# Optimization experiments

Hardware: AMD Instinct MI355X
Metric: run time of the kernel (lower is better)

The kernel has to match this reference:

```python
import jax, jax.numpy as jnp
import numpy as np

B, N_IN, D, K, N = 8, 256, 128, 1024, 4096
EMA_GAMMA = 0.99


def setup_inputs() -> dict:
    key = jax.random.key(0)
    k1, k2, k3 = jax.random.split(key, 3)
    z = jax.random.normal(k1, (B, N_IN, N), dtype=jnp.float32)
    # Conv1d(n_in, d, 1, bias=False) == a (d, n_in) matmul; xavier-ish scale
    W_lin = jax.random.normal(k2, (D, N_IN), dtype=jnp.float32) * (1.0 / np.sqrt(N_IN))
    # codebook initialized xavier_uniform with gain=10 in the original
    lim = 10.0 * np.sqrt(6.0 / (K + D))
    emb = jax.random.uniform(k3, (K, D), dtype=jnp.float32, minval=-lim, maxval=lim)
    ema_numer = emb * (1.0 - EMA_GAMMA)
    ema_denom = jnp.ones((K,), dtype=jnp.float32) * (1.0 - EMA_GAMMA)
    return {"z": z, "W_lin": W_lin, "emb": emb,
            "ema_numer": ema_numer, "ema_denom": ema_denom}


def reference(z, W_lin, emb, ema_numer, ema_denom):
    # ze: (B, d, N) -- 1x1 conv == channel matmul
    ze = jnp.einsum('bcn,dc->bdn', z, W_lin)
    sg_emb = jax.lax.stop_gradient(emb)           # codebook is stop-gradded

    # scaled L2 distance:  ||ze - q|| / (||ze|| + ||q||), shape (B, K, N)
    ze_sq = jnp.sum(ze * ze, axis=1)              # (B, N)
    q_sq = jnp.sum(sg_emb * sg_emb, axis=1)       # (K,)
    dots = jnp.einsum('bdn,kd->bkn', ze, sg_emb)  # (B, K, N)
    dist_sq = jnp.maximum(ze_sq[:, None, :] + q_sq[None, :, None] - 2.0 * dots, 0.0)
    den = jnp.sqrt(ze_sq)[:, None, :] + jnp.sqrt(q_sq)[None, :, None]
    snorm = jnp.sqrt(dist_sq) / den               # (B, K, N)

    min_ind = jnp.argmin(snorm, axis=1)           # (B, N) int
    zq = jnp.moveaxis(sg_emb[min_ind], -1, 1)     # (B, d, N)

    # ReplaceGrad: forward value = zq, gradient routed to ze (straight-through)
    zq_rg = ze + jax.lax.stop_gradient(zq - ze)

    # EMA codebook statistics (scatter-add over codebook indices)
    flat_ind = min_ind.reshape(-1)                             # (B*N,)
    ze_flat = jax.lax.stop_gradient(
        jnp.moveaxis(ze, 1, 2).reshape(-1, ze.shape[1]))       # (B*N, d)
    z_sum = jax.ops.segment_sum(ze_flat, flat_ind, num_segments=K)   # (K, d)
    n_sum = jax.ops.segment_sum(jnp.ones(flat_ind.shape, ze.dtype),
                                flat_ind, num_segments=K)            # (K,)
    ema_numer_new = EMA_GAMMA * ema_numer + (1.0 - EMA_GAMMA) * z_sum
    ema_denom_new = EMA_GAMMA * ema_denom + (1.0 - EMA_GAMMA) * n_sum
    return zq_rg, ema_numer_new, ema_denom_new
```

## Files before the change

### kernel.cpp

```cpp
#include <hip/hip_runtime.h>
#include <cmath>
#include <stdint.h>

#define B_    8
#define NIN_  256
#define D_    128
#define K_    1024
#define N_    4096
#define P_    (B_ * N_)
#define MARGIN_M 1e-4f

typedef __attribute__((ext_vector_type(8))) short bf16x8;
typedef __attribute__((ext_vector_type(4))) float f32x4;

#define WS_ZSUM   0
#define WS_CNT    524288
#define WS_FLAGC  528384
#define WS_MEMSET 532480
#define WS_OFF    532480
#define WS_QSQ    536576
#define WS_QNORM  540672
#define WS_KSTAR  544768
#define WS_RANK   675840
#define WS_PLIST  806912
#define WS_KLIST  937984
#define WS_FLIST  1069056
#define WS_WT     1200128
#define WS_ZPM    1331200
#define WS_ZESQ   18108416
#define WS_ZEN    18239488
#define WS_ZE2F   18370560
#define WS_EMB2F  43536384
#define WS_VAL1   44322816
#define WS_IDX1   46419968
#define WS_VAL2   48517120

__device__ inline unsigned short f2bf(float v) {
  union { float f; uint32_t u; } c; c.f = v;
  return (unsigned short)((c.u + 0x7FFFu + ((c.u >> 16) & 1u)) >> 16);
}
__device__ inline float bf2f(unsigned short b) {
  union { float f; uint32_t u; } c; c.u = ((uint32_t)b) << 16; return c.f;
}
__device__ inline uint32_t pack2(float a, float b, int lo) {
  unsigned short ha = f2bf(a); if (lo) ha = f2bf(a - bf2f(ha));
  unsigned short hb = f2bf(b); if (lo) hb = f2bf(b - bf2f(hb));
  return (uint32_t)ha | ((uint32_t)hb << 16);
}

__global__ __launch_bounds__(256) void prep_kernel(
    const float* __restrict__ W, const float* __restrict__ emb,
    float* __restrict__ Wt, float* __restrict__ q_sq, float* __restrict__ q_norm,
    uint4* __restrict__ emb2f)
{
  const int tid = threadIdx.x;
  const int bid = blockIdx.x;
  if (bid < 128) {
    int t = bid * 256 + tid;
    int c = t >> 7, d = t & 127;
    Wt[t] = W[d * NIN_ + c];
  } else if (bid < 132) {
    int k = (bid - 128) * 256 + tid;
    const float* e = emb + (size_t)k * D_;
    float s = 0.f;
    #pragma unroll 8
    for (int d = 0; d < D_; ++d) s = fmaf(e[d], e[d], s);
    q_sq[k] = s;
    q_norm[k] = sqrtf(s);
  } else {
    const int kt = bid - 132;
    #pragma unroll
    for (int i = 0; i < 3; ++i) {
      int f    = i * 256 + tid;
      int c    = f >> 6;
      int lane = f & 63;
      int k    = kt * 16 + (lane & 15);
      int q    = lane >> 4;
      int kk0  = c * 32 + q * 8;
      int lo   = (kk0 >> 7) == 1;
      int d0   = kk0 & 127;
      float4 v0 = *(const float4*)&emb[(size_t)k * D_ + d0];
      float4 v1 = *(const float4*)&emb[(size_t)k * D_ + d0 + 4];
      uint4 u;
      u.x = pack2(v0.x, v0.y, lo);
      u.y = pack2(v0.z, v0.w, lo);
      u.z = pack2(v1.x, v1.y, lo);
      u.w = pack2(v1.z, v1.w, lo);
      emb2f[(size_t)kt * 768 + f] = u;
    }
  }
}

__global__ __launch_bounds__(512) void ze_kernel(
    const float* __restrict__ z, const float* __restrict__ Wt,
    float* __restrict__ ze_pm, float* __restrict__ ze_sq,
    float* __restrict__ ze_norm, uint4* __restrict__ ze2f)
{
  __shared__ float tile[64][132];
  __shared__ float sqpart[8][64];
  const int t    = threadIdx.x;
  const int lane = t & 63;
  const int wv   = __builtin_amdgcn_readfirstlane(t >> 6);
  const int p    = blockIdx.x * 64 + lane;
  const int b    = p >> 12;
  const int n    = p & (N_ - 1);

  float acc[16];
  #pragma unroll
  for (int j = 0; j < 16; ++j) acc[j] = 0.f;
  const float* zp = z + (size_t)b * NIN_ * N_ + n;
  const float* wp = Wt + wv * 16;
  #pragma unroll 4
  for (int c = 0; c < NIN_; ++c) {
    float zv = zp[(size_t)c * N_];
    #pragma unroll
    for (int j = 0; j < 16; ++j)
      acc[j] = fmaf(wp[c * D_ + j], zv, acc[j]);
  }
  #pragma unroll
  for (int j = 0; j < 16; ++j) tile[lane][wv * 16 + j] = acc[j];
  float s = 0.f;
  #pragma unroll
  for (int j = 0; j < 16; ++j) s = fmaf(acc[j], acc[j], s);
  sqpart[wv][lane] = s;
  __syncthreads();
  if (wv == 0) {
    float tt = sqpart[0][lane];
    #pragma unroll
    for (int w = 1; w < 8; ++w) tt += sqpart[w][lane];
    ze_sq[p] = tt;
    ze_norm[p] = sqrtf(tt);
  }
  const int row = t >> 5;
  const int c4  = (t & 31) * 4;
  #pragma unroll
  for (int r = 0; r < 4; ++r) {
    int pr = r * 16 + row;
    float4 v = *(const float4*)&tile[pr][c4];
    *(float4*)&ze_pm[(size_t)(blockIdx.x * 64 + pr) * D_ + c4] = v;
  }
  #pragma unroll
  for (int i = 0; i < 6; ++i) {
    int f    = i * 512 + t;
    int lane_f = f & 63;
    int g    = f >> 6;
    int c    = g % 12;
    int lpt  = g / 12;
    int pl   = lpt * 16 + (lane_f & 15);
    int q    = lane_f >> 4;
    int kk0  = c * 32 + q * 8;
    int lo   = (kk0 >> 7) == 2;
    int d0   = kk0 & 127;
    float4 v0 = *(const float4*)&tile[pl][d0];
    float4 v1 = *(const float4*)&tile[pl][d0 + 4];
    uint4 u;
    u.x = pack2(v0.x, v0.y, lo);
    u.y = pack2(v0.z, v0.w, lo);
    u.z = pack2(v1.x, v1.y, lo);
    u.w = pack2(v1.z, v1.w, lo);
    ze2f[((size_t)(blockIdx.x * 4 + lpt) * 12 + c) * 64 + lane_f] = u;
  }
}

__global__ __launch_bounds__(512, 2) void mfma_argmin_kernel(
    const uint4* __restrict__ ze2f, const uint4* __restrict__ emb2f,
    const float* __restrict__ ze_sq, const float* __restrict__ ze_norm,
    const float* __restrict__ q_sq, const float* __restrict__ q_norm,
    float* __restrict__ val1, int* __restrict__ idx1, float* __restrict__ val2)
{
  __shared__ uint4 As[2][512];
  __shared__ uint4 Bs[2][1024];
  const int tid  = threadIdx.x;
  const int lane = tid & 63;
  const int tw   = tid >> 6;
  const int kb   = blockIdx.x & 3;
  const int pb   = blockIdx.x >> 2;
  const int wm   = tw & 1;
  const int wn   = tw >> 1;

  const uint4* a_base  = ze2f + ((size_t)(pb * 8 + tw) * 12) * 64 + lane;
  const uint4* b_base0 = emb2f + ((size_t)(kb * 16 + tw) * 12) * 64 + lane;
  const uint4* b_base1 = emb2f + ((size_t)(kb * 16 + tw + 8) * 12) * 64 + lane;

  f32x4 acc[4][4];
  #pragma unroll
  for (int i = 0; i < 4; ++i)
    #pragma unroll
    for (int j = 0; j < 4; ++j) acc[i][j] = (f32x4){0.f, 0.f, 0.f, 0.f};

  uint4 pa = a_base[0], pb0 = b_base0[0], pb1 = b_base1[0];
  for (int c = 0; c < 12; ++c) {
    const int buf = c & 1;
    As[buf][tid] = pa;
    Bs[buf][tid] = pb0;
    Bs[buf][512 + tid] = pb1;
    __syncthreads();
    if (c + 1 < 12) {
      pa  = a_base[(c + 1) * 64];
      pb0 = b_base0[(c + 1) * 64];
      pb1 = b_base1[(c + 1) * 64];
    }
    uint4 afr[4], bfr[4];
    #pragma unroll
    for (int i = 0; i < 4; ++i) afr[i] = As[buf][(wm * 4 + i) * 64 + lane];
    #pragma unroll
    for (int j = 0; j < 4; ++j) bfr[j] = Bs[buf][(wn * 4 + j) * 64 + lane];
    #pragma unroll
    for (int i = 0; i < 4; ++i) {
      union { uint4 u; bf16x8 h; } au; au.u = afr[i];
      #pragma unroll
      for (int j = 0; j < 4; ++j) {
        union { uint4 u; bf16x8 h; } bu; bu.u = bfr[j];
        acc[i][j] = __builtin_amdgcn_mfma_f32_16x16x32_bf16(au.h, bu.h,
                                                            acc[i][j], 0, 0, 0);
      }
    }
  }

  const int col = lane & 15;
  const int q   = lane >> 4;
  float qsq_l[4], qn_l[4]; int kg[4];
  #pragma unroll
  for (int j = 0; j < 4; ++j) {
    kg[j]    = kb * 256 + wn * 64 + j * 16 + col;
    qsq_l[j] = q_sq[kg[j]];
    qn_l[j]  = q_norm[kg[j]];
  }
  const int g = kb * 4 + wn;
  #pragma unroll
  for (int i = 0; i < 4; ++i) {
    const int pbase = pb * 128 + wm * 64 + i * 16 + q * 4;
    f32x4 zs = *(const f32x4*)&ze_sq[pbase];
    f32x4 zn = *(const f32x4*)&ze_norm[pbase];
    float m1r[4], m2r[4]; int k1r[4];
    #pragma unroll
    for (int r = 0; r < 4; ++r) { m1r[r] = 1e30f; m2r[r] = 1e30f; k1r[r] = 0; }
    #pragma unroll
    for (int j = 0; j < 4; ++j) {
      #pragma unroll
      for (int r = 0; r < 4; ++r) {
        float dsq = fmaxf(zs[r] + qsq_l[j] - 2.0f * acc[i][j][r], 0.0f);
        float den = zn[r] + qn_l[j];
        float rd  = __builtin_amdgcn_rcpf(den);
        float m   = dsq * rd * rd;
        bool take = m < m1r[r];
        float loser = take ? m1r[r] : m;
        if (take) { m1r[r] = m; k1r[r] = kg[j]; }
        m2r[r] = fminf(m2r[r], loser);
      }
    }
    #pragma unroll
    for (int ms = 1; ms <= 8; ms <<= 1) {
      #pragma unroll
      for (int r = 0; r < 4; ++r) {
        float om1 = __shfl_xor(m1r[r], ms);
        int   ok1 = __shfl_xor(k1r[r], ms);
        float om2 = __shfl_xor(m2r[r], ms);
        bool take = (om1 < m1r[r]) || (om1 == m1r[r] && ok1 < k1r[r]);
        float loser = take ? m1r[r] : om1;
        if (take) { m1r[r] = om1; k1r[r] = ok1; }
        m2r[r] = fminf(fminf(m2r[r], om2), loser);
      }
    }
    if (col == 0) {
      const size_t o = (size_t)g * P_ + pbase;
      *(float4*)&val1[o] = make_float4(m1r[0], m1r[1], m1r[2], m1r[3]);
      *(int4*)&idx1[o]   = make_int4(k1r[0], k1r[1], k1r[2], k1r[3]);
      *(float4*)&val2[o] = make_float4(m2r[0], m2r[1], m2r[2], m2r[3]);
    }
  }
}

__global__ __launch_bounds__(256) void resolve_kernel(
    const float* __restrict__ val1, const int* __restrict__ idx1,
    const float* __restrict__ val2, int* __restrict__ kstar,
    int* __restrict__ rank, int* __restrict__ counts,
    int* __restrict__ flaglist, int* __restrict__ flagcnt)
{
  const int p = blockIdx.x * 256 + threadIdx.x;
  float m1 = 1e30f, m2 = 1e30f; int k1 = 0;
  #pragma unroll
  for (int g = 0; g < 16; ++g) {
    float v1 = val1[(size_t)g * P_ + p];
    int   i1 = idx1[(size_t)g * P_ + p];
    float v2 = val2[(size_t)g * P_ + p];
    bool take = v1 < m1;
    float loser = take ? m1 : v1;
    if (take) { m1 = v1; k1 = i1; }
    m2 = fminf(fminf(m2, v2), loser);
  }
  kstar[p] = k1;
  if (m2 - m1 <= MARGIN_M) {
    int s = atomicAdd(flagcnt, 1);
    flaglist[s] = p;
  } else {
    rank[p] = atomicAdd(&counts[k1], 1);
  }
}

__global__ __launch_bounds__(256) void fallback_kernel(
    const float* __restrict__ ze_pm, const float* __restrict__ emb,
    const float* __restrict__ ze_sq, const float* __restrict__ ze_norm,
    const float* __restrict__ q_sq, const float* __restrict__ q_norm,
    const int* __restrict__ flaglist, const int* __restrict__ flagcnt,
    int* __restrict__ kstar, int* __restrict__ rank, int* __restrict__ counts)
{
  __shared__ float zlds[128];
  __shared__ float wbs[4];
  __shared__ int   wbk[4];
  const int tid  = threadIdx.x;
  const int lane = tid & 63;
  const int w    = tid >> 6;
  const int cnt  = *flagcnt;
  for (int i = blockIdx.x; i < cnt; i += gridDim.x) {
    const int p = flaglist[i];
    __syncthreads();
    if (tid < 128) zlds[tid] = ze_pm[(size_t)p * D_ + tid];
    __syncthreads();
    const float zsq = ze_sq[p], zn = ze_norm[p];
    float bs = 1e30f; int bk = 0;
    #pragma unroll
    for (int tt = 0; tt < 4; ++tt) {
      const int k = (w * 4 + tt) * 64 + lane;
      const float* e = emb + (size_t)k * D_;
      float dot = 0.f;
      #pragma unroll 8
      for (int d = 0; d < D_; ++d)
        dot = fmaf(zlds[d], e[d], dot);
      float dsq = fmaxf(fmaf(-2.0f, dot, zsq + q_sq[k]), 0.0f);
      float sn  = sqrtf(dsq) / (zn + q_norm[k]);
      if (sn < bs) { bs = sn; bk = k; }
    }
    #pragma unroll
    for (int m = 1; m <= 32; m <<= 1) {
      float ov = __shfl_xor(bs, m);
      int   ok = __shfl_xor(bk, m);
      if (ov < bs || (ov == bs && ok < bk)) { bs = ov; bk = ok; }
    }
    if (lane == 0) { wbs[w] = bs; wbk[w] = bk; }
    __syncthreads();
    if (tid == 0) {
      float fb = wbs[0]; int fk = wbk[0];
      #pragma unroll
      for (int ww = 1; ww < 4; ++ww) {
        if (wbs[ww] < fb) { fb = wbs[ww]; fk = wbk[ww]; }
      }
      kstar[p] = fk;
      rank[p] = atomicAdd(&counts[fk], 1);
    }
  }
}

__global__ __launch_bounds__(1024) void prefix_kernel(
    const int* __restrict__ counts, const float* __restrict__ ema_denom,
    int* __restrict__ offsets, float* __restrict__ out_den)
{
  __shared__ int s[1024];
  const int t = threadIdx.x;
  const int c = counts[t];
  s[t] = c;
  __syncthreads();
  for (int off = 1; off < 1024; off <<= 1) {
    int v = (t >= off) ? s[t - off] : 0;
    __syncthreads();
    s[t] += v;
    __syncthreads();
  }
  offsets[t] = s[t] - c;
  out_den[t] = 0.99f * ema_denom[t] + 0.01f * (float)c;
}

__global__ __launch_bounds__(256) void scatter_kernel(
    const int* __restrict__ kstar, const int* __restrict__ rank,
    const int* __restrict__ offsets, int* __restrict__ pos_list,
    int* __restrict__ k_list)
{
  const int p = blockIdx.x * 256 + threadIdx.x;
  const int k = kstar[p];
  const int slot = offsets[k] + rank[p];
  pos_list[slot] = p;
  k_list[slot] = k;
}

__global__ __launch_bounds__(512) void zq_kernel(
    const float* __restrict__ ze_pm, const float* __restrict__ emb,
    const int* __restrict__ kstar, float* __restrict__ out)
{
  const int tid = threadIdx.x;
  const int lane = tid & 63;
  const int w = __builtin_amdgcn_readfirstlane(tid >> 6);
  const int p = blockIdx.x * 64 + lane;
  const int b = p >> 12;
  const int n = p & (N_ - 1);
  const int kst = kstar[p];
  const float* zr = ze_pm + (size_t)p * D_ + w * 16;
  const float* ek = emb + (size_t)kst * D_ + w * 16;
  float* op = out + (size_t)b * D_ * N_ + (size_t)(w * 16) * N_ + n;
  float4 zv[4], ev[4];
  #pragma unroll
  for (int r = 0; r < 4; ++r) {
    zv[r] = *(const float4*)&zr[r * 4];
    ev[r] = *(const float4*)&ek[r * 4];
  }
  #pragma unroll
  for (int r = 0; r < 4; ++r) {
    const float* zc = (const float*)&zv[r];
    const float* ec = (const float*)&ev[r];
    #pragma unroll
    for (int jj = 0; jj < 4; ++jj) {
      float zev = zc[jj];
      op[(size_t)(r * 4 + jj) * N_] = zev + (ec[jj] - zev);
    }
  }
}

__global__ __launch_bounds__(128) void gsum_kernel(
    const float* __restrict__ ze_pm, const int* __restrict__ pos_list,
    const int* __restrict__ k_list, float* __restrict__ z_sum)
{
  const int d  = threadIdx.x;
  const int i0 = blockIdx.x * 32;
  int   kprev = -1;
  float acc = 0.f;
  #pragma unroll
  for (int ii = 0; ii < 32; ++ii) {
    int p = pos_list[i0 + ii];
    int k = k_list[i0 + ii];
    if (k != kprev) {
      if (kprev >= 0) atomicAdd(&z_sum[(size_t)kprev * D_ + d], acc);
      acc = 0.f;
      kprev = k;
    }
    acc += ze_pm[(size_t)p * D_ + d];
  }
  if (kprev >= 0) atomicAdd(&z_sum[(size_t)kprev * D_ + d], acc);
}

__global__ __launch_bounds__(256) void finalize_num_kernel(
    const float* __restrict__ ema_numer, const float* __restrict__ z_sum,
    float* __restrict__ out)
{
  const int t = blockIdx.x * 256 + threadIdx.x;
  float* out_num = out + (size_t)B_ * D_ * N_;
  out_num[t] = 0.99f * ema_numer[t] + 0.01f * z_sum[t];
}

extern "C" void kernel_launch(void* const* d_in, const int* in_sizes, int n_in,
                              void* d_out, int out_size, void* d_ws, size_t ws_size,
                              hipStream_t stream)
{
  (void)in_sizes; (void)n_in; (void)out_size; (void)ws_size;
  const float* z         = (const float*)d_in[0];
  const float* W         = (const float*)d_in[1];
  const float* emb       = (const float*)d_in[2];
  const float* ema_numer = (const float*)d_in[3];
  const float* ema_denom = (const float*)d_in[4];
  float* out = (float*)d_out;
  char*  ws  = (char*)d_ws;
  float* z_sum   = (float*)(ws + WS_ZSUM);
  int*   counts  = (int*)(ws + WS_CNT);
  int*   flagcnt = (int*)(ws + WS_FLAGC);
  int*   offsets = (int*)(ws + WS_OFF);
  float* q_sq    = (float*)(ws + WS_QSQ);
  float* q_norm  = (float*)(ws + WS_QNORM);
  int*   kstar   = (int*)(ws + WS_KSTAR);
  int*   rank    = (int*)(ws + WS_RANK);
  int*   plist   = (int*)(ws + WS_PLIST);
  int*   klist   = (int*)(ws + WS_KLIST);
  int*   flist   = (int*)(ws + WS_FLIST);
  float* Wt      = (float*)(ws + WS_WT);
  float* ze_pm   = (float*)(ws + WS_ZPM);
  float* ze_sq   = (float*)(ws + WS_ZESQ);
  float* ze_norm = (float*)(ws + WS_ZEN);
  uint4* ze2f    = (uint4*)(ws + WS_ZE2F);
  uint4* emb2f   = (uint4*)(ws + WS_EMB2F);
  float* val1    = (float*)(ws + WS_VAL1);
  int*   idx1    = (int*)(ws + WS_IDX1);
  float* val2    = (float*)(ws + WS_VAL2);
  float* out_den = out + (size_t)B_ * D_ * N_ + K_ * D_;

  hipMemsetAsync(ws, 0, WS_MEMSET, stream);

  prep_kernel<<<196, 256, 0, stream>>>(W, emb, Wt, q_sq, q_norm, emb2f);
  ze_kernel<<<P_ / 64, 512, 0, stream>>>(z, Wt, ze_pm, ze_sq, ze_norm, ze2f);
  mfma_argmin_kernel<<<1024, 512, 0, stream>>>(ze2f, emb2f, ze_sq, ze_norm,
                                               q_sq, q_norm, val1, idx1, val2);
  resolve_kernel<<<P_ / 256, 256, 0, stream>>>(val1, idx1, val2, kstar,
                                               rank, counts, flist, flagcnt);
  fallback_kernel<<<1024, 256, 0, stream>>>(ze_pm, emb, ze_sq, ze_norm,
                                            q_sq, q_norm, flist, flagcnt,
                                            kstar, rank, counts);
  prefix_kernel<<<1, 1024, 0, stream>>>(counts, ema_denom, offsets, out_den);
  scatter_kernel<<<P_ / 256, 256, 0, stream>>>(kstar, rank, offsets, plist, klist);
  zq_kernel<<<P_ / 64, 512, 0, stream>>>(ze_pm, emb, kstar, out);
  gsum_kernel<<<P_ / 32, 128, 0, stream>>>(ze_pm, plist, klist, z_sum);
  finalize_num_kernel<<<K_ * D_ / 256, 256, 0, stream>>>(ema_numer, z_sum, out);
}
```

Before: 261.2 us.

## Pack argmin index into distance mantissa and load tiles directly into LDS

The argmin kernel now swaps operand roles so the codebook becomes the MFMA A operand. It packs the code index into the low 10 mantissa bits of the score, which turns the argmin into plain fminf/fmaxf reductions with fewer shuffles and drops the idx1 buffer. Global tiles are copied straight into LDS with global_load_lds instead of staging through registers, and block indexing is reordered for cache locality. Truncating the mantissa perturbs the scores, so the ambiguity margin is widened to send more near-ties to the exact fallback path, which may increase fallback work.

```diff
diff --git a/kernel.cpp b/kernel.cpp
--- a/kernel.cpp
+++ b/kernel.cpp
@@ -8,10 +8,17 @@
 #define K_    1024
 #define N_    4096
 #define P_    (B_ * N_)
-#define MARGIN_M 1e-4f
+#define MARGIN_M 4e-4f
 
 typedef __attribute__((ext_vector_type(8))) short bf16x8;
 typedef __attribute__((ext_vector_type(4))) float f32x4;
+
+#define GLOBAL_AS __attribute__((address_space(1)))
+#define LDS_AS    __attribute__((address_space(3)))
+__device__ __forceinline__ void gll16(const void* g, void* l) {
+  __builtin_amdgcn_global_load_lds((const GLOBAL_AS void*)g, (LDS_AS void*)l,
+                                   16, 0, 0);
+}
 
 #define WS_ZSUM   0
 #define WS_CNT    524288
@@ -32,8 +39,7 @@
 #define WS_ZE2F   18370560
 #define WS_EMB2F  43536384
 #define WS_VAL1   44322816
-#define WS_IDX1   46419968
-#define WS_VAL2   48517120
+#define WS_VAL2   46419968
 
 __device__ inline unsigned short f2bf(float v) {
   union { float f; uint32_t u; } c; c.f = v;
@@ -166,21 +172,22 @@
     const uint4* __restrict__ ze2f, const uint4* __restrict__ emb2f,
     const float* __restrict__ ze_sq, const float* __restrict__ ze_norm,
     const float* __restrict__ q_sq, const float* __restrict__ q_norm,
-    float* __restrict__ val1, int* __restrict__ idx1, float* __restrict__ val2)
-{
-  __shared__ uint4 As[2][512];
-  __shared__ uint4 Bs[2][1024];
+    float* __restrict__ val1, float* __restrict__ val2)
+{
+  __shared__ uint4 As[2][1024];
+  __shared__ uint4 Bs[2][512];
   const int tid  = threadIdx.x;
   const int lane = tid & 63;
   const int tw   = tid >> 6;
-  const int kb   = blockIdx.x & 3;
-  const int pb   = blockIdx.x >> 2;
+  const int bid  = blockIdx.x;
+  const int kb   = (bid >> 3) & 3;
+  const int pb   = (bid & 7) + (bid >> 5) * 8;
+  const int wn   = tw >> 1;
   const int wm   = tw & 1;
-  const int wn   = tw >> 1;
-
-  const uint4* a_base  = ze2f + ((size_t)(pb * 8 + tw) * 12) * 64 + lane;
-  const uint4* b_base0 = emb2f + ((size_t)(kb * 16 + tw) * 12) * 64 + lane;
-  const uint4* b_base1 = emb2f + ((size_t)(kb * 16 + tw + 8) * 12) * 64 + lane;
+
+  const uint4* gA0 = emb2f + ((size_t)(kb * 16 + tw) * 12) * 64 + lane;
+  const uint4* gA1 = emb2f + ((size_t)(kb * 16 + tw + 8) * 12) * 64 + lane;
+  const uint4* gB  = ze2f  + ((size_t)(pb * 8 + tw) * 12) * 64 + lane;
 
   f32x4 acc[4][4];
   #pragma unroll
@@ -188,23 +195,22 @@
     #pragma unroll
     for (int j = 0; j < 4; ++j) acc[i][j] = (f32x4){0.f, 0.f, 0.f, 0.f};
 
-  uint4 pa = a_base[0], pb0 = b_base0[0], pb1 = b_base1[0];
+  gll16(gA0, &As[0][tw * 64 + lane]);
+  gll16(gA1, &As[0][(tw + 8) * 64 + lane]);
+  gll16(gB,  &Bs[0][tw * 64 + lane]);
   for (int c = 0; c < 12; ++c) {
     const int buf = c & 1;
-    As[buf][tid] = pa;
-    Bs[buf][tid] = pb0;
-    Bs[buf][512 + tid] = pb1;
     __syncthreads();
     if (c + 1 < 12) {
-      pa  = a_base[(c + 1) * 64];
-      pb0 = b_base0[(c + 1) * 64];
-      pb1 = b_base1[(c + 1) * 64];
+      gll16(gA0 + (c + 1) * 64, &As[buf ^ 1][tw * 64 + lane]);
+      gll16(gA1 + (c + 1) * 64, &As[buf ^ 1][(tw + 8) * 64 + lane]);
+      gll16(gB  + (c + 1) * 64, &Bs[buf ^ 1][tw * 64 + lane]);
     }
     uint4 afr[4], bfr[4];
     #pragma unroll
-    for (int i = 0; i < 4; ++i) afr[i] = As[buf][(wm * 4 + i) * 64 + lane];
-    #pragma unroll
-    for (int j = 0; j < 4; ++j) bfr[j] = Bs[buf][(wn * 4 + j) * 64 + lane];
+    for (int i = 0; i < 4; ++i) afr[i] = As[buf][(wn * 4 + i) * 64 + lane];
+    #pragma unroll
+    for (int j = 0; j < 4; ++j) bfr[j] = Bs[buf][(wm * 4 + j) * 64 + lane];
     #pragma unroll
     for (int i = 0; i < 4; ++i) {
       union { uint4 u; bf16x8 h; } au; au.u = afr[i];
@@ -219,76 +225,63 @@
 
   const int col = lane & 15;
   const int q   = lane >> 4;
-  float qsq_l[4], qn_l[4]; int kg[4];
+  const int cb  = kb * 256 + wn * 64;
+  const int g   = kb * 4 + wn;
+  f32x4 qsq4[4], qn4[4];
+  #pragma unroll
+  for (int i = 0; i < 4; ++i) {
+    qsq4[i] = *(const f32x4*)&q_sq[cb + i * 16 + q * 4];
+    qn4[i]  = *(const f32x4*)&q_norm[cb + i * 16 + q * 4];
+  }
   #pragma unroll
   for (int j = 0; j < 4; ++j) {
-    kg[j]    = kb * 256 + wn * 64 + j * 16 + col;
-    qsq_l[j] = q_sq[kg[j]];
-    qn_l[j]  = q_norm[kg[j]];
-  }
-  const int g = kb * 4 + wn;
-  #pragma unroll
-  for (int i = 0; i < 4; ++i) {
-    const int pbase = pb * 128 + wm * 64 + i * 16 + q * 4;
-    f32x4 zs = *(const f32x4*)&ze_sq[pbase];
-    f32x4 zn = *(const f32x4*)&ze_norm[pbase];
-    float m1r[4], m2r[4]; int k1r[4];
-    #pragma unroll
-    for (int r = 0; r < 4; ++r) { m1r[r] = 1e30f; m2r[r] = 1e30f; k1r[r] = 0; }
-    #pragma unroll
-    for (int j = 0; j < 4; ++j) {
+    const int pos = pb * 128 + wm * 64 + j * 16 + col;
+    const float zsq = ze_sq[pos];
+    const float zn  = ze_norm[pos];
+    float u1 = 1e30f, u2 = 1e30f;
+    #pragma unroll
+    for (int i = 0; i < 4; ++i) {
       #pragma unroll
       for (int r = 0; r < 4; ++r) {
-        float dsq = fmaxf(zs[r] + qsq_l[j] - 2.0f * acc[i][j][r], 0.0f);
-        float den = zn[r] + qn_l[j];
-        float rd  = __builtin_amdgcn_rcpf(den);
+        float dsq = fmaxf(zsq + qsq4[i][r] - 2.0f * acc[i][j][r], 0.0f);
+        float rd  = __builtin_amdgcn_rcpf(zn + qn4[i][r]);
         float m   = dsq * rd * rd;
-        bool take = m < m1r[r];
-        float loser = take ? m1r[r] : m;
-        if (take) { m1r[r] = m; k1r[r] = kg[j]; }
-        m2r[r] = fminf(m2r[r], loser);
+        union { float f; uint32_t u; } mu; mu.f = m;
+        mu.u = (mu.u & 0xFFFFFC00u) | (uint32_t)(cb + i * 16 + q * 4 + r);
+        float lo = fminf(u1, mu.f), hi = fmaxf(u1, mu.f);
+        u1 = lo; u2 = fminf(u2, hi);
       }
     }
     #pragma unroll
-    for (int ms = 1; ms <= 8; ms <<= 1) {
-      #pragma unroll
-      for (int r = 0; r < 4; ++r) {
-        float om1 = __shfl_xor(m1r[r], ms);
-        int   ok1 = __shfl_xor(k1r[r], ms);
-        float om2 = __shfl_xor(m2r[r], ms);
-        bool take = (om1 < m1r[r]) || (om1 == m1r[r] && ok1 < k1r[r]);
-        float loser = take ? m1r[r] : om1;
-        if (take) { m1r[r] = om1; k1r[r] = ok1; }
-        m2r[r] = fminf(fminf(m2r[r], om2), loser);
-      }
-    }
-    if (col == 0) {
-      const size_t o = (size_t)g * P_ + pbase;
-      *(float4*)&val1[o] = make_float4(m1r[0], m1r[1], m1r[2], m1r[3]);
-      *(int4*)&idx1[o]   = make_int4(k1r[0], k1r[1], k1r[2], k1r[3]);
-      *(float4*)&val2[o] = make_float4(m2r[0], m2r[1], m2r[2], m2r[3]);
+    for (int ms = 16; ms <= 32; ms <<= 1) {
+      float o1 = __shfl_xor(u1, ms);
+      float o2 = __shfl_xor(u2, ms);
+      float lo = fminf(u1, o1), hi = fmaxf(u1, o1);
+      u1 = lo; u2 = fminf(fminf(u2, o2), hi);
+    }
+    if (q == 0) {
+      val1[(size_t)g * P_ + pos] = u1;
+      val2[(size_t)g * P_ + pos] = u2;
     }
   }
 }
 
 __global__ __launch_bounds__(256) void resolve_kernel(
-    const float* __restrict__ val1, const int* __restrict__ idx1,
-    const float* __restrict__ val2, int* __restrict__ kstar,
-    int* __restrict__ rank, int* __restrict__ counts,
+    const float* __restrict__ val1, const float* __restrict__ val2,
+    int* __restrict__ kstar, int* __restrict__ rank, int* __restrict__ counts,
     int* __restrict__ flaglist, int* __restrict__ flagcnt)
 {
   const int p = blockIdx.x * 256 + threadIdx.x;
-  float m1 = 1e30f, m2 = 1e30f; int k1 = 0;
+  float m1 = 1e30f, m2 = 1e30f;
   #pragma unroll
   for (int g = 0; g < 16; ++g) {
     float v1 = val1[(size_t)g * P_ + p];
-    int   i1 = idx1[(size_t)g * P_ + p];
     float v2 = val2[(size_t)g * P_ + p];
-    bool take = v1 < m1;
-    float loser = take ? m1 : v1;
-    if (take) { m1 = v1; k1 = i1; }
-    m2 = fminf(fminf(m2, v2), loser);
-  }
+    float lo = fminf(m1, v1), hi = fmaxf(m1, v1);
+    m1 = lo; m2 = fminf(fminf(m2, v2), hi);
+  }
+  union { float f; uint32_t u; } mu; mu.f = m1;
+  const int k1 = (int)(mu.u & 1023u);
   kstar[p] = k1;
   if (m2 - m1 <= MARGIN_M) {
     int s = atomicAdd(flagcnt, 1);
@@ -475,7 +468,6 @@
   uint4* ze2f    = (uint4*)(ws + WS_ZE2F);
   uint4* emb2f   = (uint4*)(ws + WS_EMB2F);
   float* val1    = (float*)(ws + WS_VAL1);
-  int*   idx1    = (int*)(ws + WS_IDX1);
   float* val2    = (float*)(ws + WS_VAL2);
   float* out_den = out + (size_t)B_ * D_ * N_ + K_ * D_;
 
@@ -484,8 +476,8 @@
   prep_kernel<<<196, 256, 0, stream>>>(W, emb, Wt, q_sq, q_norm, emb2f);
   ze_kernel<<<P_ / 64, 512, 0, stream>>>(z, Wt, ze_pm, ze_sq, ze_norm, ze2f);
   mfma_argmin_kernel<<<1024, 512, 0, stream>>>(ze2f, emb2f, ze_sq, ze_norm,
-                                               q_sq, q_norm, val1, idx1, val2);
-  resolve_kernel<<<P_ / 256, 256, 0, stream>>>(val1, idx1, val2, kstar,
+                                               q_sq, q_norm, val1, val2);
+  resolve_kernel<<<P_ / 256, 256, 0, stream>>>(val1, val2, kstar,
                                                rank, counts, flist, flagcnt);
   fallback_kernel<<<1024, 256, 0, stream>>>(ze_pm, emb, ze_sq, ze_norm,
                                             q_sq, q_norm, flist, flagcnt,
```

After: 268.9 us. +3.0%, slower.
